# Kernel optimization log

Hardware: AMD Instinct MI355X
Metric: run time of the kernel (lower is better)

The kernel has to match this reference:

```python
import jax, jax.numpy as jnp
from jax import lax
import numpy as np

H = 64  # hiddenSize
I = 9   # inputSize

def _init_lstm_params(key, in_dim, hidden):
    k = 1.0 / np.sqrt(hidden)
    ks = jax.random.split(key, 4)
    w_ih = jax.random.uniform(ks[0], (4 * hidden, in_dim), minval=-k, maxval=k, dtype=jnp.float32)
    w_hh = jax.random.uniform(ks[1], (4 * hidden, hidden), minval=-k, maxval=k, dtype=jnp.float32)
    b_ih = jax.random.uniform(ks[2], (4 * hidden,), minval=-k, maxval=k, dtype=jnp.float32)
    b_hh = jax.random.uniform(ks[3], (4 * hidden,), minval=-k, maxval=k, dtype=jnp.float32)
    return w_ih, w_hh, b_ih, b_hh

def setup_inputs() -> dict:
    key = jax.random.key(0)
    kx, k0, k1, kl = jax.random.split(key, 4)
    x = jax.random.normal(kx, (4096, 336, I), dtype=jnp.float32)
    w_ih0, w_hh0, b_ih0, b_hh0 = _init_lstm_params(k0, I, H)
    w_ih1, w_hh1, b_ih1, b_hh1 = _init_lstm_params(k1, H, H)
    klw, klb = jax.random.split(kl)
    k = 1.0 / np.sqrt(H)
    w_lin = jax.random.uniform(klw, (1, H), minval=-k, maxval=k, dtype=jnp.float32)
    b_lin = jax.random.uniform(klb, (1,), minval=-k, maxval=k, dtype=jnp.float32)
    return {"x": x, "w_ih0": w_ih0, "w_hh0": w_hh0, "b_ih0": b_ih0, "b_hh0": b_hh0,
            "w_ih1": w_ih1, "w_hh1": w_hh1, "b_ih1": b_ih1, "b_hh1": b_hh1,
            "w_lin": w_lin, "b_lin": b_lin}

def _lstm_layer(x_seq, w_ih, w_hh, b_ih, b_hh):
    # x_seq: [B, T, D] -> hidden sequence [B, T, H]. PyTorch gate order: i, f, g, o.
    B = x_seq.shape[0]
    hidden = w_hh.shape[1]
    # Precompute input contribution for all timesteps in one GEMM.
    pre = jnp.einsum('btd,gd->btg', x_seq, w_ih) + b_ih + b_hh  # [B, T, 4H]
    pre_t = jnp.swapaxes(pre, 0, 1)  # [T, B, 4H]

    def step(carry, p):
        h, c = carry
        gates = p + h @ w_hh.T  # [B, 4H]
        i, f, g, o = jnp.split(gates, 4, axis=-1)
        i = jax.nn.sigmoid(i)
        f = jax.nn.sigmoid(f)
        g = jnp.tanh(g)
        o = jax.nn.sigmoid(o)
        c = f * c + i * g
        h = o * jnp.tanh(c)
        return (h, c), h

    h0 = jnp.zeros((B, hidden), dtype=x_seq.dtype)
    c0 = jnp.zeros((B, hidden), dtype=x_seq.dtype)
    _, hs = lax.scan(step, (h0, c0), pre_t)
    return jnp.swapaxes(hs, 0, 1)  # [B, T, H]

def reference(x, w_ih0, w_hh0, b_ih0, b_hh0, w_ih1, w_hh1, b_ih1, b_hh1, w_lin, b_lin):
    h1 = _lstm_layer(x, w_ih0, w_hh0, b_ih0, b_hh0)     # layer 1 (dropout inactive in eval)
    h2 = _lstm_layer(h1, w_ih1, w_hh1, b_ih1, b_hh1)    # layer 2
    last = h2[:, -1, :]                                  # [B, H]
    out = jax.nn.sigmoid(last @ w_lin.T + b_lin)         # [B, 1]
    return out
```

## Files before the change

kernel.cpp:

```cpp
#include <hip/hip_runtime.h>
#include <hip/hip_bf16.h>
#include <stdint.h>


typedef __attribute__((ext_vector_type(8))) short s16x8;
typedef __attribute__((ext_vector_type(4))) short s16x4;
typedef __attribute__((ext_vector_type(4))) float f32x4;

#define MFMA_BF16 __builtin_amdgcn_mfma_f32_16x16x32_bf16
#define LOG2E     1.4426950408889634f
#define TWO_LOG2E 2.8853900817779268f

__device__ __forceinline__ short f2bf(float f) {
    uint32_t u = __builtin_bit_cast(uint32_t, f);
    u += 0x7fffu + ((u >> 16) & 1u);
    return (short)(u >> 16);
}

__device__ __forceinline__ s16x4 pack_bf16x4(float a, float b, float c, float d) {
    union { uint32_t u[2]; s16x4 s; } r;
    asm("v_cvt_pk_bf16_f32 %0, %1, %2" : "=v"(r.u[0]) : "v"(a), "v"(b));
    asm("v_cvt_pk_bf16_f32 %0, %1, %2" : "=v"(r.u[1]) : "v"(c), "v"(d));
    return r.s;
}

__device__ __forceinline__ float rcp1p2(float t) {
    return __builtin_amdgcn_rcpf(1.0f + __builtin_amdgcn_exp2f(t));
}

__global__ __launch_bounds__(512, 1)
void lstm_fused(const float* __restrict__ x,
                const float* __restrict__ w_ih0, const float* __restrict__ w_hh0,
                const float* __restrict__ b_ih0, const float* __restrict__ b_hh0,
                const float* __restrict__ w_ih1, const float* __restrict__ w_hh1,
                const float* __restrict__ b_ih1, const float* __restrict__ b_hh1,
                const float* __restrict__ w_lin, const float* __restrict__ b_lin,
                float* __restrict__ out)
{
    __shared__ __align__(16) short xs[16 * 512];
    __shared__ __align__(16) short h0s[2][16 * 64];
    __shared__ __align__(16) short h1s[16 * 64];
    __shared__ float red[4][16];

    const int tid  = threadIdx.x;
    const int w    = tid >> 6;
    const int role = w >> 2;
    const int wl   = w & 3;
    const int l    = tid & 63;
    const int bcol = l & 15;
    const int q    = l >> 4;
    const int b0   = blockIdx.x * 16;

    for (int i = tid; i < 16 * 512; i += 512) xs[i] = 0;
    for (int i = tid; i < 16 * 64; i += 512) {
        h0s[0][i] = 0; h0s[1][i] = 0; h1s[i] = 0;
    }
    __syncthreads();

    const float scm[4] = { -LOG2E, -LOG2E, TWO_LOG2E, -LOG2E };

    s16x8 aW[4][4];
    f32x4 bias[4];
    #pragma unroll
    for (int m = 0; m < 4; ++m) {
        const int R = m * 64 + wl * 16 + bcol;
        const float sc = scm[m];
        if (role == 0) {
            #pragma unroll
            for (int r = 0; r < 8; ++r) {
                int k = q * 8 + r;
                aW[m][0][r] = (k < 9) ? f2bf(w_ih0[R * 9 + k] * sc) : (short)0;
            }
            #pragma unroll
            for (int kf = 0; kf < 2; ++kf) {
                const float* p = w_hh0 + R * 64 + kf * 32 + q * 8;
                #pragma unroll
                for (int r = 0; r < 8; ++r) aW[m][1 + kf][r] = f2bf(p[r] * sc);
            }
            #pragma unroll
            for (int r = 0; r < 8; ++r) aW[m][3][r] = 0;
            #pragma unroll
            for (int r = 0; r < 4; ++r) {
                int G = m * 64 + wl * 16 + q * 4 + r;
                bias[m][r] = (b_ih0[G] + b_hh0[G]) * sc;
            }
        } else {
            #pragma unroll
            for (int kf = 0; kf < 4; ++kf) {
                int ks = kf * 32 + q * 8;
                const float* p = (ks < 64) ? (w_ih1 + R * 64 + ks)
                                           : (w_hh1 + R * 64 + (ks - 64));
                #pragma unroll
                for (int r = 0; r < 8; ++r) aW[m][kf][r] = f2bf(p[r] * sc);
            }
            #pragma unroll
            for (int r = 0; r < 4; ++r) {
                int G = m * 64 + wl * 16 + q * 4 + r;
                bias[m][r] = (b_ih1[G] + b_hh1[G]) * sc;
            }
        }
    }

    f32x4 c  = {0.f, 0.f, 0.f, 0.f};
    f32x4 hq = {0.f, 0.f, 0.f, 0.f};
    f32x4 accL1[4];
    #pragma unroll
    for (int m = 0; m < 4; ++m) accL1[m] = (f32x4){0.f, 0.f, 0.f, 0.f};

    const int hrd0 = bcol * 64 + (((q    ) ^ (bcol & 7)) << 3);
    const int hrd1 = bcol * 64 + (((4 + q) ^ (bcol & 7)) << 3);
    const int hwr  = bcol * 64 + (((wl * 2 + (q >> 1)) ^ (bcol & 7)) << 3)
                   + ((q & 1) << 2);
    const int xrd  = bcol * 32 + ((q ^ (bcol & 3)) << 3);

    const int    ld_b = (tid & 255) >> 4, ld_t = tid & 15;
    const float* xrow = x + (size_t)(b0 + ld_b) * (336 * 9) + ld_t * 9;
    const int    xs_wr_base = ld_t * 512 + ld_b * 32;
    const int    xswzw = (ld_b & 3) << 3;

    #pragma unroll 1
    for (int i = 0; i <= 337; ++i) {
        if ((i & 15) == 0 && i < 336) {
            if (tid < 256) {
                const float* xp = xrow + (size_t)i * 9;
                #pragma unroll
                for (int d = 0; d < 9; ++d)
                    xs[(xs_wr_base + d) ^ xswzw] = f2bf(xp[d]);
            }
            __syncthreads();
        }

        f32x4 acc0[4];
        if (role == 0) {
            if (i <= 335) {
                s16x8 bx = *(const s16x8*)&xs[(i & 15) * 512 + xrd];
                const short* h0r = h0s[(i & 1) ^ 1];
                s16x8 ba = *(const s16x8*)&h0r[hrd0];
                s16x8 bb = *(const s16x8*)&h0r[hrd1];
                #pragma unroll
                for (int m = 0; m < 4; ++m) acc0[m] = MFMA_BF16(aW[m][0], bx, bias[m], 0, 0, 0);
                #pragma unroll
                for (int m = 0; m < 4; ++m) acc0[m] = MFMA_BF16(aW[m][1], ba, acc0[m], 0, 0, 0);
                #pragma unroll
                for (int m = 0; m < 4; ++m) acc0[m] = MFMA_BF16(aW[m][2], bb, acc0[m], 0, 0, 0);
            }
        } else {
            if (i >= 2) {
                #pragma unroll
                for (int r = 0; r < 4; ++r) {
                    float iv = rcp1p2(accL1[0][r]);
                    float fv = rcp1p2(accL1[1][r]);
                    float gv = fmaf(-2.f, rcp1p2(accL1[2][r]), 1.f);
                    float ov = rcp1p2(accL1[3][r]);
                    float cc = fv * c[r] + iv * gv;
                    c[r] = cc;
                    hq[r] = ov * fmaf(-2.f, rcp1p2(cc * TWO_LOG2E), 1.f);
                }
                *(s16x4*)&h1s[hwr] = pack_bf16x4(hq[0], hq[1], hq[2], hq[3]);
            }
        }
        __syncthreads();

        if (role == 0) {
            if (i <= 335) {
                #pragma unroll
                for (int r = 0; r < 4; ++r) {
                    float iv = rcp1p2(acc0[0][r]);
                    float fv = rcp1p2(acc0[1][r]);
                    float gv = fmaf(-2.f, rcp1p2(acc0[2][r]), 1.f);
                    float ov = rcp1p2(acc0[3][r]);
                    float cc = fv * c[r] + iv * gv;
                    c[r] = cc;
                    hq[r] = ov * fmaf(-2.f, rcp1p2(cc * TWO_LOG2E), 1.f);
                }
                short* h0w = h0s[i & 1];
                *(s16x4*)&h0w[hwr] = pack_bf16x4(hq[0], hq[1], hq[2], hq[3]);
            }
        } else {
            if (i >= 1 && i <= 336) {
                const short* h0r = h0s[(i & 1) ^ 1];
                s16x8 ba  = *(const s16x8*)&h0r[hrd0];
                s16x8 bb  = *(const s16x8*)&h0r[hrd1];
                s16x8 b1a = *(const s16x8*)&h1s[hrd0];
                s16x8 b1b = *(const s16x8*)&h1s[hrd1];
                #pragma unroll
                for (int m = 0; m < 4; ++m) accL1[m] = MFMA_BF16(aW[m][0], ba,  bias[m], 0, 0, 0);
                #pragma unroll
                for (int m = 0; m < 4; ++m) accL1[m] = MFMA_BF16(aW[m][1], bb,  accL1[m], 0, 0, 0);
                #pragma unroll
                for (int m = 0; m < 4; ++m) accL1[m] = MFMA_BF16(aW[m][2], b1a, accL1[m], 0, 0, 0);
                #pragma unroll
                for (int m = 0; m < 4; ++m) accL1[m] = MFMA_BF16(aW[m][3], b1b, accL1[m], 0, 0, 0);
            }
        }
        __syncthreads();
    }

    if (role == 1) {
        float part = hq[0] * w_lin[wl * 16 + q * 4 + 0]
                   + hq[1] * w_lin[wl * 16 + q * 4 + 1]
                   + hq[2] * w_lin[wl * 16 + q * 4 + 2]
                   + hq[3] * w_lin[wl * 16 + q * 4 + 3];
        part += __shfl_xor(part, 16, 64);
        part += __shfl_xor(part, 32, 64);
        if (q == 0) red[wl][bcol] = part;
    }
    __syncthreads();
    if (tid < 16) {
        float s = red[0][tid] + red[1][tid] + red[2][tid] + red[3][tid] + b_lin[0];
        out[b0 + tid] = rcp1p2(-s * LOG2E);
    }
}

extern "C" void kernel_launch(void* const* d_in, const int* in_sizes, int n_in,
                              void* d_out, int out_size, void* d_ws, size_t ws_size,
                              hipStream_t stream) {
    const float* x     = (const float*)d_in[0];
    const float* w_ih0 = (const float*)d_in[1];
    const float* w_hh0 = (const float*)d_in[2];
    const float* b_ih0 = (const float*)d_in[3];
    const float* b_hh0 = (const float*)d_in[4];
    const float* w_ih1 = (const float*)d_in[5];
    const float* w_hh1 = (const float*)d_in[6];
    const float* b_ih1 = (const float*)d_in[7];
    const float* b_hh1 = (const float*)d_in[8];
    const float* w_lin = (const float*)d_in[9];
    const float* b_lin = (const float*)d_in[10];

    lstm_fused<<<dim3(256), dim3(512), 0, stream>>>(
        x, w_ih0, w_hh0, b_ih0, b_hh0,
        w_ih1, w_hh1, b_ih1, b_hh1,
        w_lin, b_lin, (float*)d_out);
}
```

Baseline: 301.2 us.

## Merge both LSTM layers into each wave instead of splitting waves by layer

Before, the 512-thread block had two sets of four waves, one per layer. Now each of four waves holds the weights for both layers and runs layer 0 and layer 1 work interleaved within the same timestep, which halves the block size. It also reuses the h0 fragments read for layer 0 as the layer-1 input. The aim is cheaper barriers and more overlap of MFMA and transcendental work inside a wave. In exchange each wave needs more registers for the weights and does serial work per step, so the latency of each step may grow.

```diff
diff --git a/kernel.cpp b/kernel.cpp
--- a/kernel.cpp
+++ b/kernel.cpp
@@ -28,7 +28,7 @@
     return __builtin_amdgcn_rcpf(1.0f + __builtin_amdgcn_exp2f(t));
 }
 
-__global__ __launch_bounds__(512, 1)
+__global__ __launch_bounds__(256, 1)
 void lstm_fused(const float* __restrict__ x,
                 const float* __restrict__ w_ih0, const float* __restrict__ w_hh0,
                 const float* __restrict__ b_ih0, const float* __restrict__ b_hh0,
@@ -44,76 +44,66 @@
 
     const int tid  = threadIdx.x;
     const int w    = tid >> 6;
-    const int role = w >> 2;
-    const int wl   = w & 3;
     const int l    = tid & 63;
     const int bcol = l & 15;
     const int q    = l >> 4;
     const int b0   = blockIdx.x * 16;
 
-    for (int i = tid; i < 16 * 512; i += 512) xs[i] = 0;
-    for (int i = tid; i < 16 * 64; i += 512) {
+    for (int i = tid; i < 16 * 512; i += 256) xs[i] = 0;
+    for (int i = tid; i < 16 * 64; i += 256) {
         h0s[0][i] = 0; h0s[1][i] = 0; h1s[i] = 0;
     }
     __syncthreads();
 
     const float scm[4] = { -LOG2E, -LOG2E, TWO_LOG2E, -LOG2E };
 
-    s16x8 aW[4][4];
-    f32x4 bias[4];
+    s16x8 aW0[4][3];
+    s16x8 aW1[4][4];
+    f32x4 bias0[4], bias1[4];
     #pragma unroll
     for (int m = 0; m < 4; ++m) {
-        const int R = m * 64 + wl * 16 + bcol;
+        const int R = m * 64 + w * 16 + bcol;
         const float sc = scm[m];
-        if (role == 0) {
-            #pragma unroll
-            for (int r = 0; r < 8; ++r) {
-                int k = q * 8 + r;
-                aW[m][0][r] = (k < 9) ? f2bf(w_ih0[R * 9 + k] * sc) : (short)0;
-            }
-            #pragma unroll
-            for (int kf = 0; kf < 2; ++kf) {
-                const float* p = w_hh0 + R * 64 + kf * 32 + q * 8;
-                #pragma unroll
-                for (int r = 0; r < 8; ++r) aW[m][1 + kf][r] = f2bf(p[r] * sc);
-            }
-            #pragma unroll
-            for (int r = 0; r < 8; ++r) aW[m][3][r] = 0;
-            #pragma unroll
-            for (int r = 0; r < 4; ++r) {
-                int G = m * 64 + wl * 16 + q * 4 + r;
-                bias[m][r] = (b_ih0[G] + b_hh0[G]) * sc;
-            }
-        } else {
-            #pragma unroll
-            for (int kf = 0; kf < 4; ++kf) {
-                int ks = kf * 32 + q * 8;
-                const float* p = (ks < 64) ? (w_ih1 + R * 64 + ks)
-                                           : (w_hh1 + R * 64 + (ks - 64));
-                #pragma unroll
-                for (int r = 0; r < 8; ++r) aW[m][kf][r] = f2bf(p[r] * sc);
-            }
-            #pragma unroll
-            for (int r = 0; r < 4; ++r) {
-                int G = m * 64 + wl * 16 + q * 4 + r;
-                bias[m][r] = (b_ih1[G] + b_hh1[G]) * sc;
-            }
-        }
-    }
-
-    f32x4 c  = {0.f, 0.f, 0.f, 0.f};
-    f32x4 hq = {0.f, 0.f, 0.f, 0.f};
+        #pragma unroll
+        for (int r = 0; r < 8; ++r) {
+            int k = q * 8 + r;
+            aW0[m][0][r] = (k < 9) ? f2bf(w_ih0[R * 9 + k] * sc) : (short)0;
+        }
+        #pragma unroll
+        for (int kf = 0; kf < 2; ++kf) {
+            const float* p = w_hh0 + R * 64 + kf * 32 + q * 8;
+            #pragma unroll
+            for (int r = 0; r < 8; ++r) aW0[m][1 + kf][r] = f2bf(p[r] * sc);
+        }
+        #pragma unroll
+        for (int kf = 0; kf < 4; ++kf) {
+            int ks = kf * 32 + q * 8;
+            const float* p = (ks < 64) ? (w_ih1 + R * 64 + ks)
+                                       : (w_hh1 + R * 64 + (ks - 64));
+            #pragma unroll
+            for (int r = 0; r < 8; ++r) aW1[m][kf][r] = f2bf(p[r] * sc);
+        }
+        #pragma unroll
+        for (int r = 0; r < 4; ++r) {
+            int G = m * 64 + w * 16 + q * 4 + r;
+            bias0[m][r] = (b_ih0[G] + b_hh0[G]) * sc;
+            bias1[m][r] = (b_ih1[G] + b_hh1[G]) * sc;
+        }
+    }
+
+    f32x4 c0 = {0.f,0.f,0.f,0.f}, c1 = {0.f,0.f,0.f,0.f};
+    f32x4 h1q = {0.f,0.f,0.f,0.f};
     f32x4 accL1[4];
     #pragma unroll
-    for (int m = 0; m < 4; ++m) accL1[m] = (f32x4){0.f, 0.f, 0.f, 0.f};
+    for (int m = 0; m < 4; ++m) accL1[m] = (f32x4){0.f,0.f,0.f,0.f};
 
     const int hrd0 = bcol * 64 + (((q    ) ^ (bcol & 7)) << 3);
     const int hrd1 = bcol * 64 + (((4 + q) ^ (bcol & 7)) << 3);
-    const int hwr  = bcol * 64 + (((wl * 2 + (q >> 1)) ^ (bcol & 7)) << 3)
+    const int hwr  = bcol * 64 + (((w * 2 + (q >> 1)) ^ (bcol & 7)) << 3)
                    + ((q & 1) << 2);
     const int xrd  = bcol * 32 + ((q ^ (bcol & 3)) << 3);
 
-    const int    ld_b = (tid & 255) >> 4, ld_t = tid & 15;
+    const int    ld_b = tid >> 4, ld_t = tid & 15;
     const float* xrow = x + (size_t)(b0 + ld_b) * (336 * 9) + ld_t * 9;
     const int    xs_wr_base = ld_t * 512 + ld_b * 32;
     const int    xswzw = (ld_b & 3) << 3;
@@ -121,89 +111,89 @@
     #pragma unroll 1
     for (int i = 0; i <= 337; ++i) {
         if ((i & 15) == 0 && i < 336) {
-            if (tid < 256) {
-                const float* xp = xrow + (size_t)i * 9;
-                #pragma unroll
-                for (int d = 0; d < 9; ++d)
-                    xs[(xs_wr_base + d) ^ xswzw] = f2bf(xp[d]);
+            const float* xp = xrow + (size_t)i * 9;
+            #pragma unroll
+            for (int d = 0; d < 9; ++d)
+                xs[(xs_wr_base + d) ^ xswzw] = f2bf(xp[d]);
+            __syncthreads();
+        }
+
+        const bool doL0 = (i <= 335);
+        const bool rdH0 = (i <= 336);
+        const bool doL1 = (i >= 1 && i <= 336);
+
+        s16x8 bx, ba, bb;
+        if (doL0) bx = *(const s16x8*)&xs[(i & 15) * 512 + xrd];
+        if (rdH0) {
+            const short* h0r = h0s[(i & 1) ^ 1];
+            ba = *(const s16x8*)&h0r[hrd0];
+            bb = *(const s16x8*)&h0r[hrd1];
+        }
+        if (i >= 2) {
+            #pragma unroll
+            for (int r = 0; r < 4; ++r) {
+                float iv = rcp1p2(accL1[0][r]);
+                float fv = rcp1p2(accL1[1][r]);
+                float gv = fmaf(-2.f, rcp1p2(accL1[2][r]), 1.f);
+                float ov = rcp1p2(accL1[3][r]);
+                float cc = fv * c1[r] + iv * gv;
+                c1[r] = cc;
+                h1q[r] = ov * fmaf(-2.f, rcp1p2(cc * TWO_LOG2E), 1.f);
             }
-            __syncthreads();
-        }
-
+            *(s16x4*)&h1s[hwr] = pack_bf16x4(h1q[0], h1q[1], h1q[2], h1q[3]);
+        }
         f32x4 acc0[4];
-        if (role == 0) {
-            if (i <= 335) {
-                s16x8 bx = *(const s16x8*)&xs[(i & 15) * 512 + xrd];
-                const short* h0r = h0s[(i & 1) ^ 1];
-                s16x8 ba = *(const s16x8*)&h0r[hrd0];
-                s16x8 bb = *(const s16x8*)&h0r[hrd1];
-                #pragma unroll
-                for (int m = 0; m < 4; ++m) acc0[m] = MFMA_BF16(aW[m][0], bx, bias[m], 0, 0, 0);
-                #pragma unroll
-                for (int m = 0; m < 4; ++m) acc0[m] = MFMA_BF16(aW[m][1], ba, acc0[m], 0, 0, 0);
-                #pragma unroll
-                for (int m = 0; m < 4; ++m) acc0[m] = MFMA_BF16(aW[m][2], bb, acc0[m], 0, 0, 0);
+        if (doL0) {
+            #pragma unroll
+            for (int m = 0; m < 4; ++m) acc0[m] = MFMA_BF16(aW0[m][0], bx, bias0[m], 0, 0, 0);
+            #pragma unroll
+            for (int m = 0; m < 4; ++m) acc0[m] = MFMA_BF16(aW0[m][1], ba, acc0[m], 0, 0, 0);
+            #pragma unroll
+            for (int m = 0; m < 4; ++m) acc0[m] = MFMA_BF16(aW0[m][2], bb, acc0[m], 0, 0, 0);
+        }
+        __syncthreads();
+
+        s16x8 b1a, b1b;
+        if (doL1) {
+            b1a = *(const s16x8*)&h1s[hrd0];
+            b1b = *(const s16x8*)&h1s[hrd1];
+        }
+        if (doL0) {
+            #pragma unroll
+            for (int r = 0; r < 4; ++r) {
+                float iv = rcp1p2(acc0[0][r]);
+                float fv = rcp1p2(acc0[1][r]);
+                float gv = fmaf(-2.f, rcp1p2(acc0[2][r]), 1.f);
+                float ov = rcp1p2(acc0[3][r]);
+                float cc = fv * c0[r] + iv * gv;
+                c0[r] = cc;
+                float hh = ov * fmaf(-2.f, rcp1p2(cc * TWO_LOG2E), 1.f);
+                acc0[0][r] = hh;
             }
-        } else {
-            if (i >= 2) {
-                #pragma unroll
-                for (int r = 0; r < 4; ++r) {
-                    float iv = rcp1p2(accL1[0][r]);
-                    float fv = rcp1p2(accL1[1][r]);
-                    float gv = fmaf(-2.f, rcp1p2(accL1[2][r]), 1.f);
-                    float ov = rcp1p2(accL1[3][r]);
-                    float cc = fv * c[r] + iv * gv;
-                    c[r] = cc;
-                    hq[r] = ov * fmaf(-2.f, rcp1p2(cc * TWO_LOG2E), 1.f);
-                }
-                *(s16x4*)&h1s[hwr] = pack_bf16x4(hq[0], hq[1], hq[2], hq[3]);
-            }
+            short* h0w = h0s[i & 1];
+            *(s16x4*)&h0w[hwr] = pack_bf16x4(acc0[0][0], acc0[0][1], acc0[0][2], acc0[0][3]);
+        }
+        if (doL1) {
+            #pragma unroll
+            for (int m = 0; m < 4; ++m) accL1[m] = MFMA_BF16(aW1[m][0], ba,  bias1[m], 0, 0, 0);
+            #pragma unroll
+            for (int m = 0; m < 4; ++m) accL1[m] = MFMA_BF16(aW1[m][1], bb,  accL1[m], 0, 0, 0);
+            #pragma unroll
+            for (int m = 0; m < 4; ++m) accL1[m] = MFMA_BF16(aW1[m][2], b1a, accL1[m], 0, 0, 0);
+            #pragma unroll
+            for (int m = 0; m < 4; ++m) accL1[m] = MFMA_BF16(aW1[m][3], b1b, accL1[m], 0, 0, 0);
         }
         __syncthreads();
-
-        if (role == 0) {
-            if (i <= 335) {
-                #pragma unroll
-                for (int r = 0; r < 4; ++r) {
-                    float iv = rcp1p2(acc0[0][r]);
-                    float fv = rcp1p2(acc0[1][r]);
-                    float gv = fmaf(-2.f, rcp1p2(acc0[2][r]), 1.f);
-                    float ov = rcp1p2(acc0[3][r]);
-                    float cc = fv * c[r] + iv * gv;
-                    c[r] = cc;
-                    hq[r] = ov * fmaf(-2.f, rcp1p2(cc * TWO_LOG2E), 1.f);
-                }
-                short* h0w = h0s[i & 1];
-                *(s16x4*)&h0w[hwr] = pack_bf16x4(hq[0], hq[1], hq[2], hq[3]);
-            }
-        } else {
-            if (i >= 1 && i <= 336) {
-                const short* h0r = h0s[(i & 1) ^ 1];
-                s16x8 ba  = *(const s16x8*)&h0r[hrd0];
-                s16x8 bb  = *(const s16x8*)&h0r[hrd1];
-                s16x8 b1a = *(const s16x8*)&h1s[hrd0];
-                s16x8 b1b = *(const s16x8*)&h1s[hrd1];
-                #pragma unroll
-                for (int m = 0; m < 4; ++m) accL1[m] = MFMA_BF16(aW[m][0], ba,  bias[m], 0, 0, 0);
-                #pragma unroll
-                for (int m = 0; m < 4; ++m) accL1[m] = MFMA_BF16(aW[m][1], bb,  accL1[m], 0, 0, 0);
-                #pragma unroll
-                for (int m = 0; m < 4; ++m) accL1[m] = MFMA_BF16(aW[m][2], b1a, accL1[m], 0, 0, 0);
-                #pragma unroll
-                for (int m = 0; m < 4; ++m) accL1[m] = MFMA_BF16(aW[m][3], b1b, accL1[m], 0, 0, 0);
-            }
-        }
-        __syncthreads();
-    }
-
-    if (role == 1) {
-        float part = hq[0] * w_lin[wl * 16 + q * 4 + 0]
-                   + hq[1] * w_lin[wl * 16 + q * 4 + 1]
-                   + hq[2] * w_lin[wl * 16 + q * 4 + 2]
-                   + hq[3] * w_lin[wl * 16 + q * 4 + 3];
+    }
+
+    {
+        float part = h1q[0] * w_lin[w * 16 + q * 4 + 0]
+                   + h1q[1] * w_lin[w * 16 + q * 4 + 1]
+                   + h1q[2] * w_lin[w * 16 + q * 4 + 2]
+                   + h1q[3] * w_lin[w * 16 + q * 4 + 3];
         part += __shfl_xor(part, 16, 64);
         part += __shfl_xor(part, 32, 64);
-        if (q == 0) red[wl][bcol] = part;
+        if (q == 0) red[w][bcol] = part;
     }
     __syncthreads();
     if (tid < 16) {
@@ -227,7 +217,7 @@
     const float* w_lin = (const float*)d_in[9];
     const float* b_lin = (const float*)d_in[10];
 
-    lstm_fused<<<dim3(256), dim3(512), 0, stream>>>(
+    lstm_fused<<<dim3(256), dim3(256), 0, stream>>>(
         x, w_ih0, w_hh0, b_ih0, b_hh0,
         w_ih1, w_hh1, b_ih1, b_hh1,
         w_lin, b_lin, (float*)d_out);
```

After: 398.0 us. 1.32x slower.
